# Kernel tuning notes

Measured on AMD Instinct MI355X. Metric: run time of the kernel, lower is better.

Reference implementation:

```python
import jax, jax.numpy as jnp
import numpy as np

EMBED = 256
HEADS = 8
N, L, S = 4, 128, 64


def setup_inputs() -> dict:
    key = jax.random.key(0)
    ks = jax.random.split(key, 9)
    values = jax.random.normal(ks[0], (N, L, S, EMBED), dtype=jnp.float32)
    keys_ = jax.random.normal(ks[1], (N, L, S, EMBED), dtype=jnp.float32)
    query = jax.random.normal(ks[2], (N, L, S, EMBED), dtype=jnp.float32)
    mask = jax.random.randint(ks[3], (N, 1, L, L, 1), 0, 2, dtype=jnp.int32)
    sc = 1.0 / np.sqrt(EMBED)
    Wq = jax.random.normal(ks[4], (EMBED, EMBED), dtype=jnp.float32) * sc
    Wk = jax.random.normal(ks[5], (EMBED, EMBED), dtype=jnp.float32) * sc
    Wv = jax.random.normal(ks[6], (EMBED, EMBED), dtype=jnp.float32) * sc
    Wo = jax.random.normal(ks[7], (HEADS * EMBED, EMBED), dtype=jnp.float32) * (1.0 / np.sqrt(HEADS * EMBED))
    bo = jnp.zeros((EMBED,), dtype=jnp.float32)
    return {"values": values, "keys": keys_, "query": query, "mask": mask,
            "Wq": Wq, "Wk": Wk, "Wv": Wv, "Wo": Wo, "bo": bo}


def reference(values, keys, query, mask, Wq, Wk, Wv, Wo, bo):
    n, q_len, s_len, d = query.shape
    k_len = keys.shape[1]
    h = HEADS
    # Per-head projections share one weight (expand happens BEFORE Linear in
    # the original), so compute each projection once and broadcast over heads.
    q = jnp.einsum('nqsd,de->nqse', query, Wq)   # [N,Q,S,D]
    k = jnp.einsum('nksd,de->nkse', keys, Wk)    # [N,K,S,D]
    v = jnp.einsum('nksd,de->nkse', values, Wv)  # [N,K,S,D]
    # energy: nqshd,nkshd->nhqks ; identical across h pre-mask
    energy = jnp.einsum('nqsd,nksd->nqks', q, k)            # [N,Q,K,S]
    energy = jnp.broadcast_to(energy[:, None], (n, h, q_len, k_len, s_len))
    energy = jnp.where(mask == 0, jnp.float32(-1e20), energy)
    attn = jax.nn.softmax(energy / jnp.sqrt(jnp.float32(d)), axis=3)  # over K
    # out: nhqls,nlshd->nqshd
    out = jnp.einsum('nhqks,nksd->nqshd', attn, v)
    out = out.reshape(n, q_len, s_len, h * d)
    return out @ Wo + bo
```

## Files before the change

### kernel.cpp

```cpp
#include <hip/hip_runtime.h>
#include <hip/hip_bf16.h>


using bf16x4 = __attribute__((ext_vector_type(4))) __bf16;
using bf16x8 = __attribute__((ext_vector_type(8))) __bf16;
using f32x4  = __attribute__((ext_vector_type(4))) float;

#define MFMA(a, b, c) __builtin_amdgcn_mfma_f32_16x16x32_bf16((a), (b), (c), 0, 0, 0)

__device__ __forceinline__ bf16x8 cvt8(float4 f0, float4 f1) {
  bf16x8 a;
  a[0]=(__bf16)f0.x; a[1]=(__bf16)f0.y; a[2]=(__bf16)f0.z; a[3]=(__bf16)f0.w;
  a[4]=(__bf16)f1.x; a[5]=(__bf16)f1.y; a[6]=(__bf16)f1.z; a[7]=(__bf16)f1.w;
  return a;
}

__global__ __launch_bounds__(256) void prep_wosum(
    const float* __restrict__ Wo, float* __restrict__ wosum) {
  int eo = threadIdx.x, e2 = blockIdx.x;
  float s = 0.f;
#pragma unroll
  for (int h = 0; h < 8; ++h) s += Wo[((size_t)(h * 256 + e2)) * 256 + eo];
  wosum[e2 * 256 + eo] = s;
}

__global__ __launch_bounds__(512) void prep_mm(
    const float* __restrict__ Wq, const float* __restrict__ Wk,
    const float* __restrict__ Wv, const float* __restrict__ wosum,
    __bf16* __restrict__ mqk, __bf16* __restrict__ mvo) {
  const int t = threadIdx.x, lane = t & 63, w = t >> 6;
  const int lr = lane & 15, g = lane >> 4;
  const bool isV = blockIdx.y != 0;
  const float* A = isV ? Wv : Wq;
  __bf16* dst = isV ? mvo : mqk;
  bf16x8 af0[8], af1[8];
#pragma unroll
  for (int k8 = 0; k8 < 8; ++k8) {
    const float* p0 = A + (size_t)((2 * w)     * 16 + lr) * 256 + k8 * 32 + g * 8;
    const float* p1 = A + (size_t)((2 * w + 1) * 16 + lr) * 256 + k8 * 32 + g * 8;
    af0[k8] = cvt8(*(const float4*)p0, *(const float4*)(p0 + 4));
    af1[k8] = cvt8(*(const float4*)p1, *(const float4*)(p1 + 4));
  }
#pragma unroll
  for (int c = 0; c < 2; ++c) {
    int ct = blockIdx.x * 2 + c;
    bf16x8 bf[8];
    if (!isV) {
#pragma unroll
      for (int k8 = 0; k8 < 8; ++k8) {
        const float* p = Wk + (size_t)(ct * 16 + lr) * 256 + k8 * 32 + g * 8;
        bf[k8] = cvt8(*(const float4*)p, *(const float4*)(p + 4));
      }
    } else {
#pragma unroll
      for (int k8 = 0; k8 < 8; ++k8)
#pragma unroll
        for (int jj = 0; jj < 8; ++jj)
          bf[k8][jj] = (__bf16)wosum[(size_t)(k8 * 32 + g * 8 + jj) * 256 + ct * 16 + lr];
    }
    f32x4 a0 = {0.f,0.f,0.f,0.f}, a1 = {0.f,0.f,0.f,0.f};
#pragma unroll
    for (int k8 = 0; k8 < 8; ++k8) {
      a0 = MFMA(af0[k8], bf[k8], a0);
      a1 = MFMA(af1[k8], bf[k8], a1);
    }
#pragma unroll
    for (int rtl = 0; rtl < 2; ++rtl) {
      const f32x4& ac = rtl ? a1 : a0;
      bf16x4 pb;
#pragma unroll
      for (int j = 0; j < 4; ++j) pb[j] = (__bf16)ac[j];
      size_t off = (size_t)ct * 4096 + w * 512 +
                   ((2 * rtl + (g >> 1)) * 16 + lr) * 8 + 4 * (g & 1);
      *reinterpret_cast<bf16x4*>(dst + off) = pb;
    }
  }
}

__global__ __launch_bounds__(512, 2) void fused_attn(
    const float* __restrict__ Xv, const float* __restrict__ Xk,
    const float* __restrict__ Xq, const int* __restrict__ mask,
    const __bf16* __restrict__ mqk, const __bf16* __restrict__ mvo,
    const float* __restrict__ bo, float* __restrict__ out) {
  extern __shared__ char lds[];
  char* Areg = lds;
  char* Breg = lds + 65536;
  const int t = threadIdx.x, lane = t & 63, w = t >> 6;
  const int lr = lane & 15, g = lane >> 4;
  const int sl = blockIdx.x, n = sl >> 6, s = sl & 63;

  auto fill = [&](const float* __restrict__ X, float4* vr) {
#pragma unroll
    for (int i = 0; i < 8; ++i) {
      int f8 = i * 512 + t, row = f8 >> 5, c8 = f8 & 31;
      const float* src = X + ((size_t)(n * 8192 + row * 64 + s)) * 256 + c8 * 8;
      vr[2 * i]     = *reinterpret_cast<const float4*>(src);
      vr[2 * i + 1] = *reinterpret_cast<const float4*>(src + 4);
    }
  };
  auto flushv = [&](const float4* vr) {
#pragma unroll
    for (int i = 0; i < 8; ++i) {
      int f8 = i * 512 + t, row = f8 >> 5, c8 = f8 & 31;
      bf16x8 b;
      b[0]=(__bf16)vr[2*i].x;   b[1]=(__bf16)vr[2*i].y;
      b[2]=(__bf16)vr[2*i].z;   b[3]=(__bf16)vr[2*i].w;
      b[4]=(__bf16)vr[2*i+1].x; b[5]=(__bf16)vr[2*i+1].y;
      b[6]=(__bf16)vr[2*i+1].z; b[7]=(__bf16)vr[2*i+1].w;
      *reinterpret_cast<bf16x8*>(
          Areg + row * 512 + ((c8 * 16) ^ ((row & 7) << 4))) = b;
    }
  };

  {
    float4 vr[16];
    fill(Xq, vr);
    flushv(vr);
  }
  __syncthreads();

  float4 vrp[16];
  fill(Xk, vrp);
  {
    const bf16x8* wp = reinterpret_cast<const bf16x8*>(mqk);
    bf16x8 wf0[8], wf1[8];
#pragma unroll
    for (int k8 = 0; k8 < 8; ++k8) {
      wf0[k8] = wp[((2 * w)     * 8 + k8) * 64 + lane];
      wf1[k8] = wp[((2 * w + 1) * 8 + k8) * 64 + lane];
    }
#pragma unroll
    for (int ct = 0; ct < 8; ++ct) {
      bf16x8 xf[8];
#pragma unroll
      for (int k8 = 0; k8 < 8; ++k8) {
        int brow = ct * 16 + lr;
        xf[k8] = *reinterpret_cast<const bf16x8*>(
            Areg + brow * 512 + ((k8 * 64 + g * 16) ^ ((brow & 7) << 4)));
      }
      f32x4 a0 = {0.f,0.f,0.f,0.f}, a1 = {0.f,0.f,0.f,0.f};
#pragma unroll
      for (int k8 = 0; k8 < 8; ++k8) {
        a0 = MFMA(wf0[k8], xf[k8], a0);
        a1 = MFMA(wf1[k8], xf[k8], a1);
      }
      bf16x4 p0, p1;
#pragma unroll
      for (int j = 0; j < 4; ++j) { p0[j] = (__bf16)a0[j]; p1[j] = (__bf16)a1[j]; }
      *reinterpret_cast<bf16x4*>(
          Breg + ct * 8192 + w * 1024 + (lr + 16 * (0 + (g >> 1))) * 16 + (g & 1) * 8) = p0;
      *reinterpret_cast<bf16x4*>(
          Breg + ct * 8192 + w * 1024 + (lr + 16 * (2 + (g >> 1))) * 16 + (g & 1) * 8) = p1;
    }
  }
  __syncthreads();

  bf16x8 af[8];
#pragma unroll
  for (int k8 = 0; k8 < 8; ++k8)
    af[k8] = *reinterpret_cast<const bf16x8*>(Breg + w * 8192 + k8 * 1024 + lane * 16);
  flushv(vrp);
  __syncthreads();

  fill(Xv, vrp);
  int mreg[8][4];
#pragma unroll
  for (int ct = 0; ct < 8; ++ct)
#pragma unroll
    for (int j = 0; j < 4; ++j)
      mreg[ct][j] = mask[((size_t)n * 128 + w * 16 + 4 * g + j) * 128 + ct * 16 + lr];
  f32x4 sacc[8];
#pragma unroll
  for (int ct = 0; ct < 8; ++ct) {
    bf16x8 xf[8];
#pragma unroll
    for (int k8 = 0; k8 < 8; ++k8) {
      int brow = ct * 16 + lr;
      xf[k8] = *reinterpret_cast<const bf16x8*>(
          Areg + brow * 512 + ((k8 * 64 + g * 16) ^ ((brow & 7) << 4)));
    }
    f32x4 a = {0.f,0.f,0.f,0.f};
#pragma unroll
    for (int k8 = 0; k8 < 8; ++k8) a = MFMA(af[k8], xf[k8], a);
    sacc[ct] = a;
  }
  __syncthreads();
  flushv(vrp);

  float p[8][4];
#pragma unroll
  for (int j = 0; j < 4; ++j) {
    float mx = -3e38f;
#pragma unroll
    for (int ct = 0; ct < 8; ++ct) {
      float sv = mreg[ct][j] ? sacc[ct][j] * 0.0625f : -6.25e18f;
      p[ct][j] = sv;
      mx = fmaxf(mx, sv);
    }
#pragma unroll
    for (int o = 1; o < 16; o <<= 1) mx = fmaxf(mx, __shfl_xor(mx, o));
    float sum = 0.f;
#pragma unroll
    for (int ct = 0; ct < 8; ++ct) {
      float e = __expf(p[ct][j] - mx);
      p[ct][j] = e;
      sum += e;
    }
#pragma unroll
    for (int o = 1; o < 16; o <<= 1) sum += __shfl_xor(sum, o);
    float inv = 1.f / sum;
#pragma unroll
    for (int ct = 0; ct < 8; ++ct) p[ct][j] *= inv;
  }
#pragma unroll
  for (int ct = 0; ct < 8; ++ct) {
    char* bse = Breg + w * 4096 + (ct >> 1) * 1024 +
                (16 * ((ct * 2 + (lr >> 3)) & 3)) * 16 + (lr & 7) * 2;
#pragma unroll
    for (int j = 0; j < 4; ++j)
      *reinterpret_cast<__bf16*>(bse + (4 * g + j) * 16) = (__bf16)p[ct][j];
  }
  bf16x8 pa[4];
#pragma unroll
  for (int kk8 = 0; kk8 < 4; ++kk8)
    pa[kk8] = *reinterpret_cast<const bf16x8*>(Breg + w * 4096 + kk8 * 1024 + lane * 16);
  __syncthreads();

  {
    const bf16x8* wp = reinterpret_cast<const bf16x8*>(mvo);
    bf16x8 vf0[8], vf1[8];
#pragma unroll
    for (int k8 = 0; k8 < 8; ++k8) {
      vf0[k8] = wp[((2 * w)     * 8 + k8) * 64 + lane];
      vf1[k8] = wp[((2 * w + 1) * 8 + k8) * 64 + lane];
    }
#pragma unroll
    for (int ct = 0; ct < 8; ++ct) {
      bf16x8 xf[8];
#pragma unroll
      for (int k8 = 0; k8 < 8; ++k8) {
        int brow = ct * 16 + lr;
        xf[k8] = *reinterpret_cast<const bf16x8*>(
            Areg + brow * 512 + ((k8 * 64 + g * 16) ^ ((brow & 7) << 4)));
      }
      f32x4 a0 = {0.f,0.f,0.f,0.f}, a1 = {0.f,0.f,0.f,0.f};
#pragma unroll
      for (int k8 = 0; k8 < 8; ++k8) {
        a0 = MFMA(vf0[k8], xf[k8], a0);
        a1 = MFMA(vf1[k8], xf[k8], a1);
      }
      int kk8 = ct >> 1;
#pragma unroll
      for (int dth = 0; dth < 2; ++dth) {
        const f32x4& ac = dth ? a1 : a0;
        char* bse = Breg + ((2 * w + dth) * 4 + kk8) * 1024 +
                    (16 * ((ct * 2 + (lr >> 3)) & 3)) * 16 + (lr & 7) * 2;
#pragma unroll
        for (int j = 0; j < 4; ++j)
          *reinterpret_cast<__bf16*>(bse + (4 * g + j) * 16) = (__bf16)ac[j];
      }
    }
  }
  __syncthreads();

  {
    float br[16];
#pragma unroll
    for (int et = 0; et < 16; ++et) br[et] = bo[et * 16 + lr];
#pragma unroll
    for (int et = 0; et < 16; ++et) {
      bf16x8 bfr[4];
#pragma unroll
      for (int kk8 = 0; kk8 < 4; ++kk8)
        bfr[kk8] = *reinterpret_cast<const bf16x8*>(
            Breg + (et * 4 + kk8) * 1024 + lane * 16);
      f32x4 a = {0.f,0.f,0.f,0.f};
#pragma unroll
      for (int kk8 = 0; kk8 < 4; ++kk8) a = MFMA(pa[kk8], bfr[kk8], a);
#pragma unroll
      for (int j = 0; j < 4; ++j) {
        int q = w * 16 + 4 * g + j;
        out[((size_t)n * 8192 + q * 64 + s) * 256 + et * 16 + lr] = a[j] + br[et];
      }
    }
  }
}

extern "C" void kernel_launch(void* const* d_in, const int* in_sizes, int n_in,
                              void* d_out, int out_size, void* d_ws, size_t ws_size,
                              hipStream_t stream) {
  const float* values = (const float*)d_in[0];
  const float* keys   = (const float*)d_in[1];
  const float* query  = (const float*)d_in[2];
  const int*   mask   = (const int*)d_in[3];
  const float* Wq     = (const float*)d_in[4];
  const float* Wk     = (const float*)d_in[5];
  const float* Wv     = (const float*)d_in[6];
  const float* Wo     = (const float*)d_in[7];
  const float* bo     = (const float*)d_in[8];
  float* out = (float*)d_out;

  char* w = (char*)d_ws;
  float*  wosum = (float*)w;  w += 262144;
  __bf16* mqk   = (__bf16*)w; w += 131072;
  __bf16* mvo   = (__bf16*)w; w += 131072;

  prep_wosum<<<256, 256, 0, stream>>>(Wo, wosum);
  prep_mm<<<dim3(8, 2), 512, 0, stream>>>(Wq, Wk, Wv, wosum, mqk, mvo);
  fused_attn<<<256, 512, 131072, stream>>>(values, keys, query, mask,
                                           mqk, mvo, bo, out);
}
```

Before: 57.18 us.

## Double threads per block, split softmax across key halves, fuse Wo head-sum into prep

The main attention kernel now runs 1024 threads (16 waves) per block. Each wave owns one 16-column slice of the projection GEMMs, and the score/softmax stage is split across two key halves whose partial max and sum are merged through a small LDS scratch area. The separate Wo head-summing kernel is folded into prep_mm through a shared-memory transpose, and prep_mm uses twice as many blocks, removing one launch and the wosum workspace. The aim is more parallelism and latency hiding per CU, at the cost of an extra barrier, extra exp work for the merge, and higher per-block register and LDS pressure.

```diff
diff --git a/kernel.cpp b/kernel.cpp
--- a/kernel.cpp
+++ b/kernel.cpp
@@ -15,84 +15,86 @@
   return a;
 }
 
-__global__ __launch_bounds__(256) void prep_wosum(
-    const float* __restrict__ Wo, float* __restrict__ wosum) {
-  int eo = threadIdx.x, e2 = blockIdx.x;
-  float s = 0.f;
-#pragma unroll
-  for (int h = 0; h < 8; ++h) s += Wo[((size_t)(h * 256 + e2)) * 256 + eo];
-  wosum[e2 * 256 + eo] = s;
-}
-
 __global__ __launch_bounds__(512) void prep_mm(
     const float* __restrict__ Wq, const float* __restrict__ Wk,
-    const float* __restrict__ Wv, const float* __restrict__ wosum,
+    const float* __restrict__ Wv, const float* __restrict__ Wo,
     __bf16* __restrict__ mqk, __bf16* __restrict__ mvo) {
+  __shared__ float wt[256 * 17];
   const int t = threadIdx.x, lane = t & 63, w = t >> 6;
   const int lr = lane & 15, g = lane >> 4;
+  const int ct = blockIdx.x;
   const bool isV = blockIdx.y != 0;
-  const float* A = isV ? Wv : Wq;
+  const float* Aw = isV ? Wv : Wq;
   __bf16* dst = isV ? mvo : mqk;
+
   bf16x8 af0[8], af1[8];
 #pragma unroll
   for (int k8 = 0; k8 < 8; ++k8) {
-    const float* p0 = A + (size_t)((2 * w)     * 16 + lr) * 256 + k8 * 32 + g * 8;
-    const float* p1 = A + (size_t)((2 * w + 1) * 16 + lr) * 256 + k8 * 32 + g * 8;
+    const float* p0 = Aw + (size_t)((2 * w)     * 16 + lr) * 256 + k8 * 32 + g * 8;
+    const float* p1 = Aw + (size_t)((2 * w + 1) * 16 + lr) * 256 + k8 * 32 + g * 8;
     af0[k8] = cvt8(*(const float4*)p0, *(const float4*)(p0 + 4));
     af1[k8] = cvt8(*(const float4*)p1, *(const float4*)(p1 + 4));
   }
-#pragma unroll
-  for (int c = 0; c < 2; ++c) {
-    int ct = blockIdx.x * 2 + c;
-    bf16x8 bf[8];
-    if (!isV) {
-#pragma unroll
-      for (int k8 = 0; k8 < 8; ++k8) {
-        const float* p = Wk + (size_t)(ct * 16 + lr) * 256 + k8 * 32 + g * 8;
-        bf[k8] = cvt8(*(const float4*)p, *(const float4*)(p + 4));
-      }
-    } else {
-#pragma unroll
-      for (int k8 = 0; k8 < 8; ++k8)
-#pragma unroll
-        for (int jj = 0; jj < 8; ++jj)
-          bf[k8][jj] = (__bf16)wosum[(size_t)(k8 * 32 + g * 8 + jj) * 256 + ct * 16 + lr];
-    }
-    f32x4 a0 = {0.f,0.f,0.f,0.f}, a1 = {0.f,0.f,0.f,0.f};
+  bf16x8 bf[8];
+  if (!isV) {
 #pragma unroll
     for (int k8 = 0; k8 < 8; ++k8) {
-      a0 = MFMA(af0[k8], bf[k8], a0);
-      a1 = MFMA(af1[k8], bf[k8], a1);
-    }
-#pragma unroll
-    for (int rtl = 0; rtl < 2; ++rtl) {
-      const f32x4& ac = rtl ? a1 : a0;
-      bf16x4 pb;
-#pragma unroll
-      for (int j = 0; j < 4; ++j) pb[j] = (__bf16)ac[j];
-      size_t off = (size_t)ct * 4096 + w * 512 +
-                   ((2 * rtl + (g >> 1)) * 16 + lr) * 8 + 4 * (g & 1);
-      *reinterpret_cast<bf16x4*>(dst + off) = pb;
-    }
+      const float* p = Wk + (size_t)(ct * 16 + lr) * 256 + k8 * 32 + g * 8;
+      bf[k8] = cvt8(*(const float4*)p, *(const float4*)(p + 4));
+    }
+  } else {
+#pragma unroll
+    for (int i = 0; i < 8; ++i) {
+      int cell = i * 512 + t, e2 = cell >> 4, eol = cell & 15;
+      float ssum = 0.f;
+#pragma unroll
+      for (int h = 0; h < 8; ++h)
+        ssum += Wo[((size_t)(h * 256 + e2)) * 256 + ct * 16 + eol];
+      wt[e2 * 17 + eol] = ssum;
+    }
+    __syncthreads();
+#pragma unroll
+    for (int k8 = 0; k8 < 8; ++k8)
+#pragma unroll
+      for (int jj = 0; jj < 8; ++jj)
+        bf[k8][jj] = (__bf16)wt[(k8 * 32 + g * 8 + jj) * 17 + lr];
+  }
+  f32x4 a0 = {0.f,0.f,0.f,0.f}, a1 = {0.f,0.f,0.f,0.f};
+#pragma unroll
+  for (int k8 = 0; k8 < 8; ++k8) {
+    a0 = MFMA(af0[k8], bf[k8], a0);
+    a1 = MFMA(af1[k8], bf[k8], a1);
+  }
+#pragma unroll
+  for (int rtl = 0; rtl < 2; ++rtl) {
+    const f32x4& ac = rtl ? a1 : a0;
+    bf16x4 pb;
+#pragma unroll
+    for (int j = 0; j < 4; ++j) pb[j] = (__bf16)ac[j];
+    size_t off = (size_t)ct * 4096 + w * 512 +
+                 ((2 * rtl + (g >> 1)) * 16 + lr) * 8 + 4 * (g & 1);
+    *reinterpret_cast<bf16x4*>(dst + off) = pb;
   }
 }
 
-__global__ __launch_bounds__(512, 2) void fused_attn(
+__global__ __launch_bounds__(1024, 4) void fused_attn(
     const float* __restrict__ Xv, const float* __restrict__ Xk,
     const float* __restrict__ Xq, const int* __restrict__ mask,
     const __bf16* __restrict__ mqk, const __bf16* __restrict__ mvo,
     const float* __restrict__ bo, float* __restrict__ out) {
   extern __shared__ char lds[];
-  char* Areg = lds;
-  char* Breg = lds + 65536;
+  char*  A   = lds;
+  char*  B   = lds + 65536;
+  float* scr = reinterpret_cast<float*>(lds + 131072);
   const int t = threadIdx.x, lane = t & 63, w = t >> 6;
   const int lr = lane & 15, g = lane >> 4;
   const int sl = blockIdx.x, n = sl >> 6, s = sl & 63;
+  const int qt = w & 7, kh = w >> 3;
 
   auto fill = [&](const float* __restrict__ X, float4* vr) {
 #pragma unroll
-    for (int i = 0; i < 8; ++i) {
-      int f8 = i * 512 + t, row = f8 >> 5, c8 = f8 & 31;
+    for (int i = 0; i < 4; ++i) {
+      int f8 = i * 1024 + t, row = f8 >> 5, c8 = f8 & 31;
       const float* src = X + ((size_t)(n * 8192 + row * 64 + s)) * 256 + c8 * 8;
       vr[2 * i]     = *reinterpret_cast<const float4*>(src);
       vr[2 * i + 1] = *reinterpret_cast<const float4*>(src + 4);
@@ -100,76 +102,33 @@
   };
   auto flushv = [&](const float4* vr) {
 #pragma unroll
-    for (int i = 0; i < 8; ++i) {
-      int f8 = i * 512 + t, row = f8 >> 5, c8 = f8 & 31;
+    for (int i = 0; i < 4; ++i) {
+      int f8 = i * 1024 + t, row = f8 >> 5, c8 = f8 & 31;
       bf16x8 b;
       b[0]=(__bf16)vr[2*i].x;   b[1]=(__bf16)vr[2*i].y;
       b[2]=(__bf16)vr[2*i].z;   b[3]=(__bf16)vr[2*i].w;
       b[4]=(__bf16)vr[2*i+1].x; b[5]=(__bf16)vr[2*i+1].y;
       b[6]=(__bf16)vr[2*i+1].z; b[7]=(__bf16)vr[2*i+1].w;
       *reinterpret_cast<bf16x8*>(
-          Areg + row * 512 + ((c8 * 16) ^ ((row & 7) << 4))) = b;
+          A + row * 512 + ((c8 * 16) ^ ((row & 7) << 4))) = b;
     }
   };
 
+  bf16x8 wf[8];
   {
-    float4 vr[16];
+    const bf16x8* wp = reinterpret_cast<const bf16x8*>(mqk);
+#pragma unroll
+    for (int k8 = 0; k8 < 8; ++k8) wf[k8] = wp[(w * 8 + k8) * 64 + lane];
+  }
+  {
+    float4 vr[8];
     fill(Xq, vr);
     flushv(vr);
   }
   __syncthreads();
 
-  float4 vrp[16];
+  float4 vrp[8];
   fill(Xk, vrp);
-  {
-    const bf16x8* wp = reinterpret_cast<const bf16x8*>(mqk);
-    bf16x8 wf0[8], wf1[8];
-#pragma unroll
-    for (int k8 = 0; k8 < 8; ++k8) {
-      wf0[k8] = wp[((2 * w)     * 8 + k8) * 64 + lane];
-      wf1[k8] = wp[((2 * w + 1) * 8 + k8) * 64 + lane];
-    }
-#pragma unroll
-    for (int ct = 0; ct < 8; ++ct) {
-      bf16x8 xf[8];
-#pragma unroll
-      for (int k8 = 0; k8 < 8; ++k8) {
-        int brow = ct * 16 + lr;
-        xf[k8] = *reinterpret_cast<const bf16x8*>(
-            Areg + brow * 512 + ((k8 * 64 + g * 16) ^ ((brow & 7) << 4)));
-      }
-      f32x4 a0 = {0.f,0.f,0.f,0.f}, a1 = {0.f,0.f,0.f,0.f};
-#pragma unroll
-      for (int k8 = 0; k8 < 8; ++k8) {
-        a0 = MFMA(wf0[k8], xf[k8], a0);
-        a1 = MFMA(wf1[k8], xf[k8], a1);
-      }
-      bf16x4 p0, p1;
-#pragma unroll
-      for (int j = 0; j < 4; ++j) { p0[j] = (__bf16)a0[j]; p1[j] = (__bf16)a1[j]; }
-      *reinterpret_cast<bf16x4*>(
-          Breg + ct * 8192 + w * 1024 + (lr + 16 * (0 + (g >> 1))) * 16 + (g & 1) * 8) = p0;
-      *reinterpret_cast<bf16x4*>(
-          Breg + ct * 8192 + w * 1024 + (lr + 16 * (2 + (g >> 1))) * 16 + (g & 1) * 8) = p1;
-    }
-  }
-  __syncthreads();
-
-  bf16x8 af[8];
-#pragma unroll
-  for (int k8 = 0; k8 < 8; ++k8)
-    af[k8] = *reinterpret_cast<const bf16x8*>(Breg + w * 8192 + k8 * 1024 + lane * 16);
-  flushv(vrp);
-  __syncthreads();
-
-  fill(Xv, vrp);
-  int mreg[8][4];
-#pragma unroll
-  for (int ct = 0; ct < 8; ++ct)
-#pragma unroll
-    for (int j = 0; j < 4; ++j)
-      mreg[ct][j] = mask[((size_t)n * 128 + w * 16 + 4 * g + j) * 128 + ct * 16 + lr];
-  f32x4 sacc[8];
 #pragma unroll
   for (int ct = 0; ct < 8; ++ct) {
     bf16x8 xf[8];
@@ -177,22 +136,56 @@
     for (int k8 = 0; k8 < 8; ++k8) {
       int brow = ct * 16 + lr;
       xf[k8] = *reinterpret_cast<const bf16x8*>(
-          Areg + brow * 512 + ((k8 * 64 + g * 16) ^ ((brow & 7) << 4)));
-    }
+          A + brow * 512 + ((k8 * 64 + g * 16) ^ ((brow & 7) << 4)));
+    }
+    f32x4 a = {0.f,0.f,0.f,0.f};
+#pragma unroll
+    for (int k8 = 0; k8 < 8; ++k8) a = MFMA(wf[k8], xf[k8], a);
+    bf16x4 pb;
+#pragma unroll
+    for (int j = 0; j < 4; ++j) pb[j] = (__bf16)a[j];
+    *reinterpret_cast<bf16x4*>(
+        B + ct * 8192 + (w >> 1) * 1024 +
+        (lr + 16 * (2 * (w & 1) + (g >> 1))) * 16 + (g & 1) * 8) = pb;
+  }
+  __syncthreads();
+
+  bf16x8 af[8];
+#pragma unroll
+  for (int k8 = 0; k8 < 8; ++k8)
+    af[k8] = *reinterpret_cast<const bf16x8*>(B + qt * 8192 + k8 * 1024 + lane * 16);
+  flushv(vrp);
+  __syncthreads();
+
+  fill(Xv, vrp);
+  int mreg[4][4];
+#pragma unroll
+  for (int ct = 0; ct < 4; ++ct)
+#pragma unroll
+    for (int j = 0; j < 4; ++j)
+      mreg[ct][j] = mask[((size_t)n * 128 + qt * 16 + 4 * g + j) * 128 +
+                         (kh * 4 + ct) * 16 + lr];
+  f32x4 sacc[4];
+#pragma unroll
+  for (int ct = 0; ct < 4; ++ct) {
+    int brow = (kh * 4 + ct) * 16 + lr;
+    bf16x8 xf[8];
+#pragma unroll
+    for (int k8 = 0; k8 < 8; ++k8)
+      xf[k8] = *reinterpret_cast<const bf16x8*>(
+          A + brow * 512 + ((k8 * 64 + g * 16) ^ ((brow & 7) << 4)));
     f32x4 a = {0.f,0.f,0.f,0.f};
 #pragma unroll
     for (int k8 = 0; k8 < 8; ++k8) a = MFMA(af[k8], xf[k8], a);
     sacc[ct] = a;
   }
-  __syncthreads();
-  flushv(vrp);
-
-  float p[8][4];
+
+  float p[4][4], mxv[4], smv[4];
 #pragma unroll
   for (int j = 0; j < 4; ++j) {
     float mx = -3e38f;
 #pragma unroll
-    for (int ct = 0; ct < 8; ++ct) {
+    for (int ct = 0; ct < 4; ++ct) {
       float sv = mreg[ct][j] ? sacc[ct][j] * 0.0625f : -6.25e18f;
       p[ct][j] = sv;
       mx = fmaxf(mx, sv);
@@ -201,87 +194,98 @@
     for (int o = 1; o < 16; o <<= 1) mx = fmaxf(mx, __shfl_xor(mx, o));
     float sum = 0.f;
 #pragma unroll
-    for (int ct = 0; ct < 8; ++ct) {
+    for (int ct = 0; ct < 4; ++ct) {
       float e = __expf(p[ct][j] - mx);
       p[ct][j] = e;
       sum += e;
     }
 #pragma unroll
     for (int o = 1; o < 16; o <<= 1) sum += __shfl_xor(sum, o);
-    float inv = 1.f / sum;
-#pragma unroll
-    for (int ct = 0; ct < 8; ++ct) p[ct][j] *= inv;
-  }
-#pragma unroll
-  for (int ct = 0; ct < 8; ++ct) {
-    char* bse = Breg + w * 4096 + (ct >> 1) * 1024 +
-                (16 * ((ct * 2 + (lr >> 3)) & 3)) * 16 + (lr & 7) * 2;
+    mxv[j] = mx; smv[j] = sum;
+  }
+  if (lr == 0) {
+#pragma unroll
+    for (int j = 0; j < 4; ++j) {
+      scr[w * 32 + g * 8 + j * 2]     = mxv[j];
+      scr[w * 32 + g * 8 + j * 2 + 1] = smv[j];
+    }
+  }
+  __syncthreads();
+
+  {
+    int pw = w ^ 8;
+#pragma unroll
+    for (int j = 0; j < 4; ++j) {
+      float pmx = scr[pw * 32 + g * 8 + j * 2];
+      float psm = scr[pw * 32 + g * 8 + j * 2 + 1];
+      float M = fmaxf(mxv[j], pmx);
+      float tot = smv[j] * __expf(mxv[j] - M) + psm * __expf(pmx - M);
+      float scale = __expf(mxv[j] - M) / tot;
+#pragma unroll
+      for (int ct = 0; ct < 4; ++ct) p[ct][j] *= scale;
+    }
+  }
+#pragma unroll
+  for (int ct = 0; ct < 4; ++ct) {
+    int cg = kh * 4 + ct;
+    char* bse = B + qt * 4096 + (cg >> 1) * 1024 +
+                (16 * ((cg * 2 + (lr >> 3)) & 3)) * 16 + (lr & 7) * 2;
 #pragma unroll
     for (int j = 0; j < 4; ++j)
       *reinterpret_cast<__bf16*>(bse + (4 * g + j) * 16) = (__bf16)p[ct][j];
   }
-  bf16x8 pa[4];
-#pragma unroll
-  for (int kk8 = 0; kk8 < 4; ++kk8)
-    pa[kk8] = *reinterpret_cast<const bf16x8*>(Breg + w * 4096 + kk8 * 1024 + lane * 16);
-  __syncthreads();
-
+  flushv(vrp);
+  __syncthreads();
+
+  bf16x8 vf[8];
   {
     const bf16x8* wp = reinterpret_cast<const bf16x8*>(mvo);
-    bf16x8 vf0[8], vf1[8];
-#pragma unroll
-    for (int k8 = 0; k8 < 8; ++k8) {
-      vf0[k8] = wp[((2 * w)     * 8 + k8) * 64 + lane];
-      vf1[k8] = wp[((2 * w + 1) * 8 + k8) * 64 + lane];
-    }
-#pragma unroll
-    for (int ct = 0; ct < 8; ++ct) {
-      bf16x8 xf[8];
-#pragma unroll
-      for (int k8 = 0; k8 < 8; ++k8) {
-        int brow = ct * 16 + lr;
-        xf[k8] = *reinterpret_cast<const bf16x8*>(
-            Areg + brow * 512 + ((k8 * 64 + g * 16) ^ ((brow & 7) << 4)));
-      }
-      f32x4 a0 = {0.f,0.f,0.f,0.f}, a1 = {0.f,0.f,0.f,0.f};
-#pragma unroll
-      for (int k8 = 0; k8 < 8; ++k8) {
-        a0 = MFMA(vf0[k8], xf[k8], a0);
-        a1 = MFMA(vf1[k8], xf[k8], a1);
-      }
-      int kk8 = ct >> 1;
-#pragma unroll
-      for (int dth = 0; dth < 2; ++dth) {
-        const f32x4& ac = dth ? a1 : a0;
-        char* bse = Breg + ((2 * w + dth) * 4 + kk8) * 1024 +
-                    (16 * ((ct * 2 + (lr >> 3)) & 3)) * 16 + (lr & 7) * 2;
-#pragma unroll
-        for (int j = 0; j < 4; ++j)
-          *reinterpret_cast<__bf16*>(bse + (4 * g + j) * 16) = (__bf16)ac[j];
-      }
-    }
-  }
-  __syncthreads();
-
-  {
-    float br[16];
-#pragma unroll
-    for (int et = 0; et < 16; ++et) br[et] = bo[et * 16 + lr];
-#pragma unroll
-    for (int et = 0; et < 16; ++et) {
-      bf16x8 bfr[4];
-#pragma unroll
-      for (int kk8 = 0; kk8 < 4; ++kk8)
-        bfr[kk8] = *reinterpret_cast<const bf16x8*>(
-            Breg + (et * 4 + kk8) * 1024 + lane * 16);
-      f32x4 a = {0.f,0.f,0.f,0.f};
-#pragma unroll
-      for (int kk8 = 0; kk8 < 4; ++kk8) a = MFMA(pa[kk8], bfr[kk8], a);
-#pragma unroll
-      for (int j = 0; j < 4; ++j) {
-        int q = w * 16 + 4 * g + j;
-        out[((size_t)n * 8192 + q * 64 + s) * 256 + et * 16 + lr] = a[j] + br[et];
-      }
+#pragma unroll
+    for (int k8 = 0; k8 < 8; ++k8) vf[k8] = wp[(w * 8 + k8) * 64 + lane];
+  }
+  bf16x8 pa[4];
+#pragma unroll
+  for (int kk8 = 0; kk8 < 4; ++kk8)
+    pa[kk8] = *reinterpret_cast<const bf16x8*>(B + qt * 4096 + kk8 * 1024 + lane * 16);
+  __syncthreads();
+
+  float br[8];
+#pragma unroll
+  for (int e8 = 0; e8 < 8; ++e8) br[e8] = bo[(kh * 8 + e8) * 16 + lr];
+#pragma unroll
+  for (int ct = 0; ct < 8; ++ct) {
+    int brow = ct * 16 + lr;
+    bf16x8 xf[8];
+#pragma unroll
+    for (int k8 = 0; k8 < 8; ++k8)
+      xf[k8] = *reinterpret_cast<const bf16x8*>(
+          A + brow * 512 + ((k8 * 64 + g * 16) ^ ((brow & 7) << 4)));
+    f32x4 a = {0.f,0.f,0.f,0.f};
+#pragma unroll
+    for (int k8 = 0; k8 < 8; ++k8) a = MFMA(vf[k8], xf[k8], a);
+    char* bse = B + w * 4096 + (ct >> 1) * 1024 +
+                (16 * ((ct * 2 + (lr >> 3)) & 3)) * 16 + (lr & 7) * 2;
+#pragma unroll
+    for (int j = 0; j < 4; ++j)
+      *reinterpret_cast<__bf16*>(bse + (4 * g + j) * 16) = (__bf16)a[j];
+  }
+  __syncthreads();
+
+#pragma unroll
+  for (int e8 = 0; e8 < 8; ++e8) {
+    int et = kh * 8 + e8;
+    bf16x8 bfr[4];
+#pragma unroll
+    for (int kk8 = 0; kk8 < 4; ++kk8)
+      bfr[kk8] = *reinterpret_cast<const bf16x8*>(
+          B + et * 4096 + kk8 * 1024 + lane * 16);
+    f32x4 a = {0.f,0.f,0.f,0.f};
+#pragma unroll
+    for (int kk8 = 0; kk8 < 4; ++kk8) a = MFMA(pa[kk8], bfr[kk8], a);
+#pragma unroll
+    for (int j = 0; j < 4; ++j) {
+      int q = qt * 16 + 4 * g + j;
+      out[((size_t)n * 8192 + q * 64 + s) * 256 + et * 16 + lr] = a[j] + br[e8];
     }
   }
 }
@@ -301,12 +305,10 @@
   float* out = (float*)d_out;
 
   char* w = (char*)d_ws;
-  float*  wosum = (float*)w;  w += 262144;
-  __bf16* mqk   = (__bf16*)w; w += 131072;
-  __bf16* mvo   = (__bf16*)w; w += 131072;
-
-  prep_wosum<<<256, 256, 0, stream>>>(Wo, wosum);
-  prep_mm<<<dim3(8, 2), 512, 0, stream>>>(Wq, Wk, Wv, wosum, mqk, mvo);
-  fused_attn<<<256, 512, 131072, stream>>>(values, keys, query, mask,
-                                           mqk, mvo, bo, out);
+  __bf16* mqk = (__bf16*)w; w += 131072;
+  __bf16* mvo = (__bf16*)w; w += 131072;
+
+  prep_mm<<<dim3(16, 2), 512, 0, stream>>>(Wq, Wk, Wv, Wo, mqk, mvo);
+  fused_attn<<<256, 1024, 133120, stream>>>(values, keys, query, mask,
+                                            mqk, mvo, bo, out);
 }
```

Measured after the change: 55.59 us. -2.8%, faster.
